# Performance work log

Measured on AMD Instinct MI355X. Metric: run time of the kernel, lower is better.

## Reference

```python
import jax, jax.numpy as jnp
import numpy as np

RES, RES_, STRIDE = 28, 14, 2
H, KD, AR = 8, 16, 4
SCALE = KD ** -0.5
EPS = 1e-5


def make_bias_idxs(res=RES, res_=RES_, stride=STRIDE):
    pts = [(i, j) for i in range(res) for j in range(res)]
    pts_ = [(i, j) for i in range(res_) for j in range(res_)]
    offs, idxs = {}, []
    for p1 in pts_:
        for p2 in pts:
            off = (abs(p1[0] * stride - p2[0]), abs(p1[1] * stride - p2[1]))
            if off not in offs:
                offs[off] = len(offs)
            idxs.append(offs[off])
    return np.array(idxs, dtype=np.int32).reshape(len(pts_), len(pts)), len(offs)


def setup_inputs() -> dict:
    key = jax.random.key(0)
    ks = jax.random.split(key, 16)
    idxs, n_off = make_bias_idxs()  # n_off == 784
    B, N, C = 128, RES * RES, 256
    d_kv, d_q, d_p, d_pin = 640, 128, 384, 512
    return {
        "hidden_state": jax.random.normal(ks[0], (B, N, C), jnp.float32),
        "w_kv": jax.random.normal(ks[1], (d_kv, C), jnp.float32) * 0.05,
        "kv_gamma": jax.random.uniform(ks[2], (d_kv,), jnp.float32, 0.5, 1.5),
        "kv_beta": jax.random.normal(ks[3], (d_kv,), jnp.float32) * 0.1,
        "kv_mean": jax.random.normal(ks[4], (d_kv,), jnp.float32) * 0.1,
        "kv_var": jax.random.uniform(ks[5], (d_kv,), jnp.float32, 0.5, 1.5),
        "w_q": jax.random.normal(ks[6], (d_q, C), jnp.float32) * 0.05,
        "q_gamma": jax.random.uniform(ks[7], (d_q,), jnp.float32, 0.5, 1.5),
        "q_beta": jax.random.normal(ks[8], (d_q,), jnp.float32) * 0.1,
        "q_mean": jax.random.normal(ks[9], (d_q,), jnp.float32) * 0.1,
        "q_var": jax.random.uniform(ks[10], (d_q,), jnp.float32, 0.5, 1.5),
        "w_proj": jax.random.normal(ks[11], (d_p, d_pin), jnp.float32) * 0.05,
        "p_gamma": jax.random.uniform(ks[12], (d_p,), jnp.float32, 0.5, 1.5),
        "p_beta": jax.random.normal(ks[13], (d_p,), jnp.float32) * 0.1,
        "p_mean": jax.random.normal(ks[14], (d_p,), jnp.float32) * 0.1,
        "p_var": jax.random.uniform(ks[15], (d_p,), jnp.float32, 0.5, 1.5),
        "attention_biases": jax.random.normal(jax.random.fold_in(key, 99), (H, n_off), jnp.float32),
        "attention_bias_idxs": jnp.asarray(idxs),
    }


def _bn(x, gamma, beta, mean, var):
    # eval-mode BatchNorm1d over last dim
    return (x - mean) * (gamma * jax.lax.rsqrt(var + EPS)) + beta


def _hardswish(x):
    return x * jnp.clip(x + 3.0, 0.0, 6.0) * (1.0 / 6.0)


def reference(hidden_state, w_kv, kv_gamma, kv_beta, kv_mean, kv_var,
              w_q, q_gamma, q_beta, q_mean, q_var,
              w_proj, p_gamma, p_beta, p_mean, p_var,
              attention_biases, attention_bias_idxs):
    B, N, C = hidden_state.shape
    N_ = RES_ * RES_
    # kv: [B, N, 640] -> key [B,H,N,KD], value [B,H,N,AR*KD]
    kv = _bn(hidden_state @ w_kv.T, kv_gamma, kv_beta, kv_mean, kv_var)
    kv = kv.reshape(B, N, H, KD + AR * KD)
    k = jnp.transpose(kv[..., :KD], (0, 2, 1, 3))          # [B,H,N,KD]
    v = jnp.transpose(kv[..., KD:], (0, 2, 1, 3))          # [B,H,N,AR*KD]
    # strided query subsample on the spatial grid
    hs = hidden_state.reshape(B, RES, RES, C)[:, ::STRIDE, ::STRIDE].reshape(B, N_, C)
    q = _bn(hs @ w_q.T, q_gamma, q_beta, q_mean, q_var)
    q = jnp.transpose(q.reshape(B, N_, H, KD), (0, 2, 1, 3))  # [B,H,N_,KD]
    bias = attention_biases[:, attention_bias_idxs]           # [H,N_,N] gathered
    attn = jnp.einsum('bhqd,bhkd->bhqk', q, k) * SCALE + bias
    attn = jax.nn.softmax(attn, axis=-1)
    out = jnp.einsum('bhqk,bhkd->bhqd', attn, v)              # [B,H,N_,AR*KD]
    out = jnp.transpose(out, (0, 2, 1, 3)).reshape(B, N_, H * AR * KD)
    out = _bn(_hardswish(out) @ w_proj.T, p_gamma, p_beta, p_mean, p_var)
    return out
```

## Files before the change

kernel.cpp:

```cpp
#include <hip/hip_runtime.h>

typedef _Float16 f16;
typedef __attribute__((ext_vector_type(2))) _Float16 f16x2;
typedef __attribute__((ext_vector_type(4))) _Float16 f16x4;
typedef __attribute__((ext_vector_type(8))) _Float16 f16x8;
typedef __attribute__((ext_vector_type(4))) float fvec4;
typedef __attribute__((ext_vector_type(4))) float f32x4;
typedef __attribute__((ext_vector_type(16))) float f32x16;
typedef __attribute__((ext_vector_type(4))) unsigned int uint4v;

#define NKEY 784
#define NKEYP 800
#define NQ 196
#define NQP 224
#define LOG2E 1.442695041f
#define SC2   0.360673760f
#define THR2  11.5415603f

static __device__ __forceinline__ f32x4 mfma16(f16x8 a, f16x8 b, f32x4 c) {
    return __builtin_amdgcn_mfma_f32_16x16x32_f16(a, b, c, 0, 0, 0);
}
static __device__ __forceinline__ f32x16 mfma32(f16x8 a, f16x8 b, f32x16 c) {
    return __builtin_amdgcn_mfma_f32_32x32x16_f16(a, b, c, 0, 0, 0);
}
static __device__ __forceinline__ unsigned pk2(float a, float b) {
    f16x2 t; t[0] = (_Float16)a; t[1] = (_Float16)b;
    return __builtin_bit_cast(unsigned, t);
}
static __device__ __forceinline__ f32x16 z16() {
    f32x16 v;
#pragma unroll
    for (int i = 0; i < 16; ++i) v[i] = 0.f;
    return v;
}

__global__ void prep_scales_all(const float* __restrict__ kg, const float* __restrict__ kb,
                                const float* __restrict__ km, const float* __restrict__ kvv,
                                const float* __restrict__ qg, const float* __restrict__ qb,
                                const float* __restrict__ qm, const float* __restrict__ qv,
                                const float* __restrict__ pg, const float* __restrict__ pb,
                                const float* __restrict__ pm, const float* __restrict__ pv,
                                float* __restrict__ sb) {
    int i = blockIdx.x * 256 + threadIdx.x;
    if (i < 640) {
        float s = kg[i] * rsqrtf(kvv[i] + 1e-5f);
        sb[i] = s; sb[640 + i] = kb[i] - km[i] * s;
    } else if (i < 768) {
        int j = i - 640;
        float s = qg[j] * rsqrtf(qv[j] + 1e-5f);
        sb[1280 + j] = s; sb[1408 + j] = qb[j] - qm[j] * s;
    } else if (i < 1152) {
        int j = i - 768;
        float s = pg[j] * rsqrtf(pv[j] + 1e-5f);
        sb[1536 + j] = s; sb[1920 + j] = pb[j] - pm[j] * s;
    }
}

__global__ void conv_w(const float* __restrict__ wkv, const float* __restrict__ wq,
                       const float* __restrict__ wp, f16* __restrict__ out) {
    int i = blockIdx.x * 256 + threadIdx.x;
    const float* src;
    f16* dst;
    int kc, n, K;
    if (i < 20480)      { int j = i;         kc = j / 640, n = j - kc * 640; src = wkv; dst = out + (size_t)j * 8;            K = 256; }
    else if (i < 24576) { int j = i - 20480; kc = j / 128, n = j - kc * 128; src = wq;  dst = out + 163840 + (size_t)j * 8;   K = 256; }
    else                { int j = i - 24576; kc = j / 384, n = j - kc * 384; src = wp;  dst = out + 196608 + (size_t)j * 8;   K = 512; }
    const float* s = src + (size_t)n * K + kc * 8;
    fvec4 v0 = *(const fvec4*)s;
    fvec4 v1 = *(const fvec4*)(s + 4);
    f16x8 h;
    h[0] = (f16)v0[0]; h[1] = (f16)v0[1]; h[2] = (f16)v0[2]; h[3] = (f16)v0[3];
    h[4] = (f16)v1[0]; h[5] = (f16)v1[1]; h[6] = (f16)v1[2]; h[7] = (f16)v1[3];
    *(f16x8*)dst = h;
}

__global__ void prep_bias(const float* __restrict__ biases, const int* __restrict__ idxs,
                          f16* __restrict__ biasS, int n_off) {
    int tid = blockIdx.x * 256 + threadIdx.x;
    const int r = tid & 15;
    const int lane = (tid >> 4) & 63;
    const int g = tid >> 10;
    const int kbk = g % 25;
    const int tmp = g / 25;
    const int qt = tmp % 7;
    const int h = tmp / 7;
    const int q = qt * 32 + (lane & 31);
    const int key = kbk * 32 + (r & 3) + 8 * (r >> 2) + 4 * (lane >> 5);
    float v = 0.f;
    if (q < NQ && key < NKEY) v = biases[h * n_off + idxs[q * NKEY + key]] * LOG2E;
    biasS[tid] = (f16)v;
}

template <int MODE>
__global__ __launch_bounds__(256) void gemm_db(
        const void* __restrict__ Ap, const f16x8* __restrict__ Wg,
        const float* __restrict__ sc, const float* __restrict__ sh,
        void* __restrict__ OutA, f16* __restrict__ OutV) {
    constexpr int K     = (MODE == 2) ? 512 : 256;
    constexpr int KS    = K / 32;
    constexpr int CHUNK = (MODE == 2) ? 16 : 32;
    constexpr int NFR   = CHUNK / 16;
    constexpr int NT    = (MODE == 0) ? 640 : (MODE == 1 ? 128 : 384);
    constexpr int NCH   = (MODE == 0) ? 10 : (MODE == 1 ? 4 : 12);
    constexpr int UNITS = (K / 8) * CHUNK;
    constexpr int SR    = UNITS / 256;

    __shared__ f16x8 Wl[2][UNITS];

    const int t = threadIdx.x;
    const int lane = t & 63, wid = t >> 6;
    const int fr = lane & 15, kg = lane >> 4;
    const int m0 = blockIdx.x * 64;
    const int nb0 = blockIdx.y * (NCH * CHUNK);
    const int mrow = m0 + wid * 16 + fr;

    size_t arow;
    if constexpr (MODE == 1) {
        int b = mrow / 196, nn = mrow - b * 196;
        arow = (size_t)b * 784 + (nn / 14) * 56 + (nn % 14) * 2;
    } else {
        arow = (size_t)mrow;
    }
    f16x8 af[KS];
#pragma unroll
    for (int ks = 0; ks < KS; ++ks) {
        if constexpr (MODE == 2) {
            af[ks] = *(const f16x8*)((const f16*)Ap + arow * K + ks * 32 + kg * 8);
        } else {
            const float* a = (const float*)Ap + arow * 256 + ks * 32 + kg * 8;
            fvec4 v0 = *(const fvec4*)a;
            fvec4 v1 = *(const fvec4*)(a + 4);
            f16x8 hv;
            hv[0] = (f16)v0[0]; hv[1] = (f16)v0[1]; hv[2] = (f16)v0[2]; hv[3] = (f16)v0[3];
            hv[4] = (f16)v1[0]; hv[5] = (f16)v1[1]; hv[6] = (f16)v1[2]; hv[7] = (f16)v1[3];
            af[ks] = hv;
        }
    }

#pragma unroll
    for (int rr = 0; rr < SR; ++rr) {
        const int idx = rr * 256 + t;
        Wl[0][idx] = Wg[(size_t)(idx / CHUNK) * NT + nb0 + (idx % CHUNK)];
    }
    __syncthreads();

    const int rg = kg * 4;
    int cur = 0;
    for (int c = 0; c < NCH; ++c) {
        const int n0c = nb0 + c * CHUNK;

        f16x8 nx0, nx1, nx2, nx3;
        if (c + 1 < NCH) {
            const int n0n = n0c + CHUNK;
            nx0 = Wg[(size_t)((0 * 256 + t) / CHUNK) * NT + n0n + ((0 * 256 + t) % CHUNK)];
            nx1 = Wg[(size_t)((1 * 256 + t) / CHUNK) * NT + n0n + ((1 * 256 + t) % CHUNK)];
            nx2 = Wg[(size_t)((2 * 256 + t) / CHUNK) * NT + n0n + ((2 * 256 + t) % CHUNK)];
            nx3 = Wg[(size_t)((3 * 256 + t) / CHUNK) * NT + n0n + ((3 * 256 + t) % CHUNK)];
        }

        f32x4 acc[NFR];
#pragma unroll
        for (int j = 0; j < NFR; ++j) acc[j] = (f32x4){0.f, 0.f, 0.f, 0.f};
#pragma unroll
        for (int ks = 0; ks < KS; ++ks) {
            f16x8 bfr[NFR];
#pragma unroll
            for (int nf = 0; nf < NFR; ++nf)
                bfr[nf] = Wl[cur][(ks * 4 + kg) * CHUNK + nf * 16 + fr];
#pragma unroll
            for (int nf = 0; nf < NFR; ++nf)
                acc[nf] = mfma16(af[ks], bfr[nf], acc[nf]);
        }

        const int mbase = m0 + wid * 16 + rg;
#pragma unroll
        for (int nf = 0; nf < NFR; ++nf) {
            const int n = n0c + nf * 16 + fr;
            const float scn = sc[n], shn = sh[n];
            if constexpr (MODE == 0) {
                const int b = mbase / 784;
                const int nn = mbase - b * 784;
                const int hd = n / 80;
                const int cc = n - hd * 80;
                const size_t bh = (size_t)(b * 8 + hd);
                if (cc < 16) {
#pragma unroll
                    for (int r = 0; r < 4; ++r) {
                        float y = acc[nf][r] * scn + shn;
                        ((f16*)OutA)[(bh * NKEYP + nn + r) * 16 + cc] = (f16)y;
                    }
                } else {
                    const int kbk = nn >> 5, sH = (nn >> 4) & 1, kk = nn & 15;
                    f16x4 pv;
#pragma unroll
                    for (int r = 0; r < 4; ++r) pv[r] = (f16)(acc[nf][r] * scn + shn);
                    *(f16x4*)(OutV + ((bh * 25 + kbk) * 2 + sH) * 1024 + (cc - 16) * 16 + kk) = pv;
                }
            } else if constexpr (MODE == 1) {
                const int b = mbase / 196;
                const int nn = mbase - b * 196;
                const int hd = n >> 4, cc = n & 15;
                const size_t bh = (size_t)(b * 8 + hd);
#pragma unroll
                for (int r = 0; r < 4; ++r) {
                    float y = acc[nf][r] * scn + shn;
                    ((f16*)OutA)[(bh * NQP + nn + r) * 16 + cc] = (f16)y;
                }
            } else {
#pragma unroll
                for (int r = 0; r < 4; ++r) {
                    float y = acc[nf][r] * scn + shn;
                    ((float*)OutA)[(size_t)(mbase + r) * 384 + n] = y;
                }
            }
        }

        if (c + 1 < NCH) {
            Wl[cur ^ 1][0 * 256 + t] = nx0;
            Wl[cur ^ 1][1 * 256 + t] = nx1;
            Wl[cur ^ 1][2 * 256 + t] = nx2;
            Wl[cur ^ 1][3 * 256 + t] = nx3;
            __syncthreads();
            cur ^= 1;
        }
    }
}

__global__ __launch_bounds__(448) void attn_fused(const f16* __restrict__ kb,
                                                  const f16* __restrict__ vtb,
                                                  const f16* __restrict__ qw,
                                                  const f16* __restrict__ biasS,
                                                  f16* __restrict__ ao) {
    const int bh = blockIdx.x;
    const int b = bh >> 3, h = bh & 7;
    const int wid = threadIdx.x >> 6;
    const int lane = threadIdx.x & 63;
    const int l31 = lane & 31;
    const int hh = lane >> 5;
    const int q0 = wid * 32;

    const f16* kp = kb + (size_t)bh * (NKEYP * 16);
    const f16* vp = vtb + (size_t)bh * 51200;
    const f16x8 bq = *(const f16x8*)(qw + ((size_t)bh * NQP + q0 + l31) * 16 + hh * 8);
    const f16* bbase = biasS + (((size_t)(h * 7 + wid) * 25) * 64 + lane) * 16;

    float mrun = -1e30f;
    float lsum = 0.f;
    f32x16 o0 = z16(), o1 = z16();

    for (int key0 = 0; key0 < NKEY; key0 += 32) {
        const int kbi = key0 >> 5;
        f16x8 ak = *(const f16x8*)(kp + (size_t)(key0 + l31) * 16 + hh * 8);
        f32x16 s = mfma32(ak, bq, z16());
        const bool tail = (key0 + 32) > NKEY;
        const f16x8* bp = (const f16x8*)(bbase + (size_t)kbi * 1024);
        f16x8 b0 = bp[0], b1 = bp[1];
        float p[16];
        float cmax = -3.0e38f;
#pragma unroll
        for (int r = 0; r < 16; ++r) {
            const int cr = (r & 3) + ((r >> 2) << 3) + (hh << 2);
            float bv = (r < 8) ? (float)b0[r] : (float)b1[r - 8];
            float sv = s[r] * SC2 + bv;
            if (tail && (key0 + cr) >= NKEY) sv = -1e30f;
            p[r] = sv;
            cmax = fmaxf(cmax, sv);
        }
        cmax = fmaxf(cmax, __shfl_xor(cmax, 32));
        if (__any(cmax > mrun + THR2)) {
            float mnew = fmaxf(mrun, cmax);
            float f = exp2f(mrun - mnew);
            mrun = mnew;
            lsum *= f;
#pragma unroll
            for (int r = 0; r < 16; ++r) {
                const int cr = (r & 3) + ((r >> 2) << 3) + (hh << 2);
                float fr2 = __shfl(f, cr);
                o0[r] *= fr2;
                o1[r] *= fr2;
            }
        }
        float psum = 0.f;
#pragma unroll
        for (int r = 0; r < 16; ++r) {
            p[r] = exp2f(p[r] - mrun);
            psum += p[r];
        }
        lsum += psum;
        unsigned g0l = pk2(p[0], p[1]),   g0h = pk2(p[2], p[3]);
        unsigned g1l = pk2(p[4], p[5]),   g1h = pk2(p[6], p[7]);
        unsigned g2l = pk2(p[8], p[9]),   g2h = pk2(p[10], p[11]);
        unsigned g3l = pk2(p[12], p[13]), g3h = pk2(p[14], p[15]);
        __builtin_amdgcn_s_setprio(1);
        const f16* vkb = vp + (size_t)kbi * 2048;
#pragma unroll
        for (int sH = 0; sH < 2; ++sH) {
            unsigned self_lo = sH ? (hh ? g3l : g2l) : (hh ? g1l : g0l);
            unsigned self_hi = sH ? (hh ? g3h : g2h) : (hh ? g1h : g0h);
            unsigned tx_lo   = sH ? (hh ? g2l : g3l) : (hh ? g0l : g1l);
            unsigned tx_hi   = sH ? (hh ? g2h : g3h) : (hh ? g0h : g1h);
            unsigned rx_lo = __shfl_xor(tx_lo, 32);
            unsigned rx_hi = __shfl_xor(tx_hi, 32);
            uint4v w;
            w[0] = hh ? rx_lo : self_lo;
            w[1] = hh ? rx_hi : self_hi;
            w[2] = hh ? self_lo : rx_lo;
            w[3] = hh ? self_hi : rx_hi;
            f16x8 pa = __builtin_bit_cast(f16x8, w);
            const f16* vrow = vkb + sH * 1024 + l31 * 16 + hh * 8;
            f16x8 bv0 = *(const f16x8*)(vrow);
            f16x8 bv1 = *(const f16x8*)(vrow + 512);
            o0 = mfma32(pa, bv0, o0);
            o1 = mfma32(pa, bv1, o1);
        }
        __builtin_amdgcn_s_setprio(0);
    }
    lsum += __shfl_xor(lsum, 32);
    const float inv = 1.0f / lsum;
#pragma unroll
    for (int r = 0; r < 16; ++r) {
        const int cr = (r & 3) + ((r >> 2) << 3) + (hh << 2);
        const float iq = __shfl(inv, cr);
        const int qg = q0 + cr;
        if (qg < NQ) {
            float v0 = o0[r] * iq, v1 = o1[r] * iq;
            float h0 = v0 * fminf(fmaxf(v0 + 3.f, 0.f), 6.f) * (1.f / 6.f);
            float h1 = v1 * fminf(fmaxf(v1 + 3.f, 0.f), 6.f) * (1.f / 6.f);
            f16* dst = ao + ((size_t)b * NQ + qg) * 512 + h * 64 + l31;
            dst[0] = (f16)h0;
            dst[32] = (f16)h1;
        }
    }
}

extern "C" void kernel_launch(void* const* d_in, const int* in_sizes, int n_in,
                              void* d_out, int out_size, void* d_ws, size_t ws_size,
                              hipStream_t stream) {
    (void)n_in; (void)out_size; (void)ws_size;
    const float* hidden = (const float*)d_in[0];
    const float* w_kv   = (const float*)d_in[1];
    const float* w_q    = (const float*)d_in[6];
    const float* w_p    = (const float*)d_in[11];
    const float* biases = (const float*)d_in[16];
    const int*   idxs   = (const int*)d_in[17];
    const int n_off = in_sizes[16] / 8;

    char* ws = (char*)d_ws;
    const size_t OFF_K  = 0;
    const size_t OFF_V  = 26214400;
    const size_t OFF_Q  = 131072000;
    const size_t OFF_AO = 138412032;
    const size_t OFF_BT = 164102144;
    const size_t OFF_W  = 166969344;
    const size_t OFF_SC = 167755776;
    f16*   kbuf  = (f16*)(ws + OFF_K);
    f16*   vbuf  = (f16*)(ws + OFF_V);
    f16*   qbuf  = (f16*)(ws + OFF_Q);
    f16*   aobuf = (f16*)(ws + OFF_AO);
    f16*   btbuf = (f16*)(ws + OFF_BT);
    f16*   wf16  = (f16*)(ws + OFF_W);
    float* scbuf = (float*)(ws + OFF_SC);

    prep_scales_all<<<5, 256, 0, stream>>>(
        (const float*)d_in[2], (const float*)d_in[3], (const float*)d_in[4], (const float*)d_in[5],
        (const float*)d_in[7], (const float*)d_in[8], (const float*)d_in[9], (const float*)d_in[10],
        (const float*)d_in[12], (const float*)d_in[13], (const float*)d_in[14], (const float*)d_in[15],
        scbuf);
    conv_w<<<192, 256, 0, stream>>>(w_kv, w_q, w_p, wf16);
    prep_bias<<<5600, 256, 0, stream>>>(biases, idxs, btbuf, n_off);
    hipMemsetAsync(qbuf, 0, (size_t)1024 * NQP * 16 * 2, stream);
    gemm_db<0><<<dim3(1568, 2), 256, 0, stream>>>(hidden, (const f16x8*)wf16, scbuf, scbuf + 640, kbuf, vbuf);
    gemm_db<1><<<dim3(392, 1), 256, 0, stream>>>(hidden, (const f16x8*)(wf16 + 163840), scbuf + 1280, scbuf + 1408, qbuf, nullptr);
    attn_fused<<<1024, 448, 0, stream>>>(kbuf, vbuf, qbuf, btbuf, aobuf);
    gemm_db<2><<<dim3(392, 2), 256, 0, stream>>>(aobuf, (const f16x8*)(wf16 + 196608), scbuf + 1536, scbuf + 1920, d_out, nullptr);
}
```

Baseline: 222.2 us.

## Fold bias and scale into MFMA accumulator init and reorder V layout to drop shuffles

```diff
diff --git a/kernel.cpp b/kernel.cpp
--- a/kernel.cpp
+++ b/kernel.cpp
@@ -23,9 +23,8 @@
 static __device__ __forceinline__ f32x16 mfma32(f16x8 a, f16x8 b, f32x16 c) {
     return __builtin_amdgcn_mfma_f32_32x32x16_f16(a, b, c, 0, 0, 0);
 }
-static __device__ __forceinline__ unsigned pk2(float a, float b) {
-    f16x2 t; t[0] = (_Float16)a; t[1] = (_Float16)b;
-    return __builtin_bit_cast(unsigned, t);
+static __device__ __forceinline__ unsigned pkrtz(float a, float b) {
+    return __builtin_bit_cast(unsigned, __builtin_amdgcn_cvt_pkrtz(a, b));
 }
 static __device__ __forceinline__ f32x16 z16() {
     f32x16 v;
@@ -48,7 +47,8 @@
     } else if (i < 768) {
         int j = i - 640;
         float s = qg[j] * rsqrtf(qv[j] + 1e-5f);
-        sb[1280 + j] = s; sb[1408 + j] = qb[j] - qm[j] * s;
+        sb[1280 + j] = s * SC2;
+        sb[1408 + j] = (qb[j] - qm[j] * s) * SC2;
     } else if (i < 1152) {
         int j = i - 768;
         float s = pg[j] * rsqrtf(pv[j] + 1e-5f);
@@ -75,20 +75,24 @@
 }
 
 __global__ void prep_bias(const float* __restrict__ biases, const int* __restrict__ idxs,
-                          f16* __restrict__ biasS, int n_off) {
+                          float* __restrict__ biasC, int n_off) {
     int tid = blockIdx.x * 256 + threadIdx.x;
-    const int r = tid & 15;
-    const int lane = (tid >> 4) & 63;
+    const int rj = tid & 3;
+    const int lane = (tid >> 2) & 63;
+    const int rr = (tid >> 8) & 3;
     const int g = tid >> 10;
+    const int r = rr * 4 + rj;
     const int kbk = g % 25;
     const int tmp = g / 25;
     const int qt = tmp % 7;
     const int h = tmp / 7;
     const int q = qt * 32 + (lane & 31);
     const int key = kbk * 32 + (r & 3) + 8 * (r >> 2) + 4 * (lane >> 5);
-    float v = 0.f;
-    if (q < NQ && key < NKEY) v = biases[h * n_off + idxs[q * NKEY + key]] * LOG2E;
-    biasS[tid] = (f16)v;
+    float v;
+    if (key >= NKEY)  v = -1e30f;
+    else if (q < NQ)  v = biases[h * n_off + idxs[q * NKEY + key]] * LOG2E;
+    else              v = 0.f;
+    biasC[tid] = v;
 }
 
 template <int MODE>
@@ -190,11 +194,13 @@
                         ((f16*)OutA)[(bh * NKEYP + nn + r) * 16 + cc] = (f16)y;
                     }
                 } else {
-                    const int kbk = nn >> 5, sH = (nn >> 4) & 1, kk = nn & 15;
+                    const int kbk = nn >> 5, sH = (nn >> 4) & 1;
+                    const int kq = (nn >> 2) & 3;
+                    const int slot = ((((kq & 1) << 1) | (kq >> 1)) << 2) | (nn & 3);
                     f16x4 pv;
 #pragma unroll
                     for (int r = 0; r < 4; ++r) pv[r] = (f16)(acc[nf][r] * scn + shn);
-                    *(f16x4*)(OutV + ((bh * 25 + kbk) * 2 + sH) * 1024 + (cc - 16) * 16 + kk) = pv;
+                    *(f16x4*)(OutV + ((bh * 25 + kbk) * 2 + sH) * 1024 + (cc - 16) * 16 + slot) = pv;
                 }
             } else if constexpr (MODE == 1) {
                 const int b = mbase / 196;
@@ -229,7 +235,7 @@
 __global__ __launch_bounds__(448) void attn_fused(const f16* __restrict__ kb,
                                                   const f16* __restrict__ vtb,
                                                   const f16* __restrict__ qw,
-                                                  const f16* __restrict__ biasS,
+                                                  const float* __restrict__ biasC,
                                                   f16* __restrict__ ao) {
     const int bh = blockIdx.x;
     const int b = bh >> 3, h = bh & 7;
@@ -242,30 +248,31 @@
     const f16* kp = kb + (size_t)bh * (NKEYP * 16);
     const f16* vp = vtb + (size_t)bh * 51200;
     const f16x8 bq = *(const f16x8*)(qw + ((size_t)bh * NQP + q0 + l31) * 16 + hh * 8);
-    const f16* bbase = biasS + (((size_t)(h * 7 + wid) * 25) * 64 + lane) * 16;
+    const float* cb = biasC + (size_t)(h * 7 + wid) * 25 * 1024 + lane * 4;
 
     float mrun = -1e30f;
     float lsum = 0.f;
     f32x16 o0 = z16(), o1 = z16();
 
-    for (int key0 = 0; key0 < NKEY; key0 += 32) {
-        const int kbi = key0 >> 5;
-        f16x8 ak = *(const f16x8*)(kp + (size_t)(key0 + l31) * 16 + hh * 8);
-        f32x16 s = mfma32(ak, bq, z16());
-        const bool tail = (key0 + 32) > NKEY;
-        const f16x8* bp = (const f16x8*)(bbase + (size_t)kbi * 1024);
-        f16x8 b0 = bp[0], b1 = bp[1];
-        float p[16];
-        float cmax = -3.0e38f;
-#pragma unroll
-        for (int r = 0; r < 16; ++r) {
-            const int cr = (r & 3) + ((r >> 2) << 3) + (hh << 2);
-            float bv = (r < 8) ? (float)b0[r] : (float)b1[r - 8];
-            float sv = s[r] * SC2 + bv;
-            if (tail && (key0 + cr) >= NKEY) sv = -1e30f;
-            p[r] = sv;
-            cmax = fmaxf(cmax, sv);
-        }
+    for (int kbi = 0; kbi < 25; ++kbi) {
+        f16x8 ak = *(const f16x8*)(kp + (size_t)(kbi * 32 + l31) * 16 + hh * 8);
+        const float* cbk = cb + kbi * 1024;
+        fvec4 c0 = *(const fvec4*)(cbk);
+        fvec4 c1 = *(const fvec4*)(cbk + 256);
+        fvec4 c2 = *(const fvec4*)(cbk + 512);
+        fvec4 c3 = *(const fvec4*)(cbk + 768);
+        f32x16 ci;
+        ci[0] = c0[0];  ci[1] = c0[1];  ci[2] = c0[2];  ci[3] = c0[3];
+        ci[4] = c1[0];  ci[5] = c1[1];  ci[6] = c1[2];  ci[7] = c1[3];
+        ci[8] = c2[0];  ci[9] = c2[1];  ci[10] = c2[2]; ci[11] = c2[3];
+        ci[12] = c3[0]; ci[13] = c3[1]; ci[14] = c3[2]; ci[15] = c3[3];
+        f32x16 s = mfma32(ak, bq, ci);
+
+        float m0v = fmaxf(fmaxf(s[0], s[1]), fmaxf(s[2], s[3]));
+        float m1v = fmaxf(fmaxf(s[4], s[5]), fmaxf(s[6], s[7]));
+        float m2v = fmaxf(fmaxf(s[8], s[9]), fmaxf(s[10], s[11]));
+        float m3v = fmaxf(fmaxf(s[12], s[13]), fmaxf(s[14], s[15]));
+        float cmax = fmaxf(fmaxf(m0v, m1v), fmaxf(m2v, m3v));
         cmax = fmaxf(cmax, __shfl_xor(cmax, 32));
         if (__any(cmax > mrun + THR2)) {
             float mnew = fmaxf(mrun, cmax);
@@ -280,39 +287,31 @@
                 o1[r] *= fr2;
             }
         }
+        float p[16];
         float psum = 0.f;
 #pragma unroll
         for (int r = 0; r < 16; ++r) {
-            p[r] = exp2f(p[r] - mrun);
+            p[r] = exp2f(s[r] - mrun);
             psum += p[r];
         }
         lsum += psum;
-        unsigned g0l = pk2(p[0], p[1]),   g0h = pk2(p[2], p[3]);
-        unsigned g1l = pk2(p[4], p[5]),   g1h = pk2(p[6], p[7]);
-        unsigned g2l = pk2(p[8], p[9]),   g2h = pk2(p[10], p[11]);
-        unsigned g3l = pk2(p[12], p[13]), g3h = pk2(p[14], p[15]);
+        uint4v w0, w1;
+        w0[0] = pkrtz(p[0], p[1]);   w0[1] = pkrtz(p[2], p[3]);
+        w0[2] = pkrtz(p[4], p[5]);   w0[3] = pkrtz(p[6], p[7]);
+        w1[0] = pkrtz(p[8], p[9]);   w1[1] = pkrtz(p[10], p[11]);
+        w1[2] = pkrtz(p[12], p[13]); w1[3] = pkrtz(p[14], p[15]);
+        f16x8 pa0 = __builtin_bit_cast(f16x8, w0);
+        f16x8 pa1 = __builtin_bit_cast(f16x8, w1);
+        const f16* vkb = vp + (size_t)kbi * 2048 + l31 * 16 + hh * 8;
+        f16x8 bv00 = *(const f16x8*)(vkb);
+        f16x8 bv01 = *(const f16x8*)(vkb + 512);
+        f16x8 bv10 = *(const f16x8*)(vkb + 1024);
+        f16x8 bv11 = *(const f16x8*)(vkb + 1536);
         __builtin_amdgcn_s_setprio(1);
-        const f16* vkb = vp + (size_t)kbi * 2048;
-#pragma unroll
-        for (int sH = 0; sH < 2; ++sH) {
-            unsigned self_lo = sH ? (hh ? g3l : g2l) : (hh ? g1l : g0l);
-            unsigned self_hi = sH ? (hh ? g3h : g2h) : (hh ? g1h : g0h);
-            unsigned tx_lo   = sH ? (hh ? g2l : g3l) : (hh ? g0l : g1l);
-            unsigned tx_hi   = sH ? (hh ? g2h : g3h) : (hh ? g0h : g1h);
-            unsigned rx_lo = __shfl_xor(tx_lo, 32);
-            unsigned rx_hi = __shfl_xor(tx_hi, 32);
-            uint4v w;
-            w[0] = hh ? rx_lo : self_lo;
-            w[1] = hh ? rx_hi : self_hi;
-            w[2] = hh ? self_lo : rx_lo;
-            w[3] = hh ? self_hi : rx_hi;
-            f16x8 pa = __builtin_bit_cast(f16x8, w);
-            const f16* vrow = vkb + sH * 1024 + l31 * 16 + hh * 8;
-            f16x8 bv0 = *(const f16x8*)(vrow);
-            f16x8 bv1 = *(const f16x8*)(vrow + 512);
-            o0 = mfma32(pa, bv0, o0);
-            o1 = mfma32(pa, bv1, o1);
-        }
+        o0 = mfma32(pa0, bv00, o0);
+        o1 = mfma32(pa0, bv01, o1);
+        o0 = mfma32(pa1, bv10, o0);
+        o1 = mfma32(pa1, bv11, o1);
         __builtin_amdgcn_s_setprio(0);
     }
     lsum += __shfl_xor(lsum, 32);
@@ -336,7 +335,7 @@
 extern "C" void kernel_launch(void* const* d_in, const int* in_sizes, int n_in,
                               void* d_out, int out_size, void* d_ws, size_t ws_size,
                               hipStream_t stream) {
-    (void)n_in; (void)out_size; (void)ws_size;
+    (void)n_in; (void)out_size;
     const float* hidden = (const float*)d_in[0];
     const float* w_kv   = (const float*)d_in[1];
     const float* w_q    = (const float*)d_in[6];
@@ -350,16 +349,17 @@
     const size_t OFF_V  = 26214400;
     const size_t OFF_Q  = 131072000;
     const size_t OFF_AO = 138412032;
-    const size_t OFF_BT = 164102144;
-    const size_t OFF_W  = 166969344;
-    const size_t OFF_SC = 167755776;
+    const size_t OFF_W  = 164102144;
+    const size_t OFF_SC = 164888576;
+    const size_t OFF_BT = 164897792;
+    const size_t NEED   = OFF_BT + 5734400;
     f16*   kbuf  = (f16*)(ws + OFF_K);
     f16*   vbuf  = (f16*)(ws + OFF_V);
     f16*   qbuf  = (f16*)(ws + OFF_Q);
     f16*   aobuf = (f16*)(ws + OFF_AO);
-    f16*   btbuf = (f16*)(ws + OFF_BT);
     f16*   wf16  = (f16*)(ws + OFF_W);
     float* scbuf = (float*)(ws + OFF_SC);
+    float* btbuf = (ws_size >= NEED) ? (float*)(ws + OFF_BT) : (float*)d_out;
 
     prep_scales_all<<<5, 256, 0, stream>>>(
         (const float*)d_in[2], (const float*)d_in[3], (const float*)d_in[4], (const float*)d_in[5],
```

Result: faster. 213.4 us (-4.0%).
